# Kernel tuning notes

Measured on AMD Instinct MI355X. Metric: run time of the kernel, lower is better.

The kernel has to match this reference:

```python
import math
import jax, jax.numpy as jnp
from jax import lax
import numpy as np

B, DIM, H, W = 8, 256, 64, 64
D_STATE, D_CONV, EXPAND = 16, 4, 2
D_INNER = EXPAND * DIM
DT_RANK = math.ceil(DIM / 16)
POS_LEN = 16
EPS = 1e-5
GN_GROUPS = 32


def setup_inputs() -> dict:
    key = jax.random.key(0)
    ks = iter(jax.random.split(key, 24))
    rn = lambda shape, s=0.02: jax.random.normal(next(ks), shape, jnp.float32) * s
    inp = {}
    inp["x"] = jax.random.normal(next(ks), (B, DIM, H, W), jnp.float32)
    inp["pos_emb"] = rn((1, DIM, POS_LEN), 1.0)
    inp["ln_g"] = jnp.ones((DIM,), jnp.float32)
    inp["ln_b"] = jnp.zeros((DIM,), jnp.float32)
    inp["m_in_w"] = rn((2, 2 * D_INNER, DIM))
    inp["m_conv_w"] = rn((2, D_INNER, D_CONV), 0.1)
    inp["m_conv_b"] = jnp.zeros((2, D_INNER), jnp.float32)
    inp["m_xproj_w"] = rn((2, DT_RANK + 2 * D_STATE, D_INNER))
    inp["m_dt_w"] = rn((2, D_INNER, DT_RANK), 0.1)
    inp["m_dt_b"] = rn((2, D_INNER), 0.1)
    inp["m_A_log"] = jnp.tile(jnp.log(jnp.arange(1, D_STATE + 1, dtype=jnp.float32))[None, None, :], (2, D_INNER, 1))
    inp["m_D"] = jnp.ones((2, D_INNER), jnp.float32)
    inp["m_out_w"] = rn((2, DIM, D_INNER))
    inp["proj_w"] = rn((DIM, 2 * DIM))
    inp["proj_b"] = jnp.zeros((DIM,), jnp.float32)
    inp["up_dw_w"] = rn((DIM, 1, 3, 3), 0.1)
    inp["up_bn1_g"] = jnp.ones((DIM,), jnp.float32)
    inp["up_bn1_b"] = jnp.zeros((DIM,), jnp.float32)
    inp["up_pw_w"] = rn((DIM, DIM), 0.05)
    inp["up_bn2_g"] = jnp.ones((DIM,), jnp.float32)
    inp["up_bn2_b"] = jnp.zeros((DIM,), jnp.float32)
    inp["down_pw_w"] = rn((DIM, DIM), 0.05)
    inp["down_bn_g"] = jnp.ones((DIM,), jnp.float32)
    inp["down_bn_b"] = jnp.zeros((DIM,), jnp.float32)
    inp["gn_g"] = jnp.ones((DIM,), jnp.float32)
    inp["gn_b"] = jnp.zeros((DIM,), jnp.float32)
    return inp


def reference(x, pos_emb, ln_g, ln_b, m_in_w, m_conv_w, m_conv_b, m_xproj_w, m_dt_w, m_dt_b,
              m_A_log, m_D, m_out_w, proj_w, proj_b, up_dw_w, up_bn1_g, up_bn1_b, up_pw_w,
              up_bn2_g, up_bn2_b, down_pw_w, down_bn_g, down_bn_b, gn_g, gn_b):
    Bx, C, Hh, Ww = x.shape

    def ln(t):  # LayerNorm over last dim (shared self.norm)
        m = jnp.mean(t, -1, keepdims=True)
        v = jnp.mean((t - m) ** 2, -1, keepdims=True)
        return (t - m) * lax.rsqrt(v + EPS) * ln_g + ln_b

    def bn(t, g, b):  # BatchNorm2d in eval mode with default running stats (mean 0, var 1)
        return t * (g / jnp.sqrt(1.0 + EPS))[None, :, None, None] + b[None, :, None, None]

    def gn(t):  # GroupNorm(32, C), shared params (self.bn)
        Bn, Cn, Hn, Wn = t.shape
        tg = t.reshape(Bn, GN_GROUPS, Cn // GN_GROUPS, Hn, Wn)
        m = jnp.mean(tg, (2, 3, 4), keepdims=True)
        v = jnp.mean((tg - m) ** 2, (2, 3, 4), keepdims=True)
        tg = (tg - m) * lax.rsqrt(v + EPS)
        return tg.reshape(Bn, Cn, Hn, Wn) * gn_g[None, :, None, None] + gn_b[None, :, None, None]

    def interp_pos(N):  # F.interpolate(pos_embed, size=N, mode='linear', align_corners=False)
        coords = jnp.maximum((jnp.arange(N, dtype=jnp.float32) + 0.5) * (POS_LEN / N) - 0.5, 0.0)
        i0 = jnp.floor(coords).astype(jnp.int32)
        i1 = jnp.minimum(i0 + 1, POS_LEN - 1)
        wgt = coords - i0.astype(jnp.float32)
        return pos_emb[:, :, i0] * (1.0 - wgt) + pos_emb[:, :, i1] * wgt  # (1,C,N)

    def pe_branch(vals, idx, N):  # vals (B,C,N); indices interp at same size = identity
        t = vals + interp_pos(N) + idx.astype(jnp.float32)
        return ln(jnp.swapaxes(t, 1, 2))  # (B,N,C)

    def mamba(u, d):  # standard mamba_ssm selective scan; u (B,L,C)
        xz = jnp.einsum('blc,ic->bli', u, m_in_w[d])
        xh, zg = jnp.split(xz, 2, -1)
        xc = lax.conv_general_dilated(jnp.swapaxes(xh, 1, 2), m_conv_w[d][:, None, :], (1,),
                                      [(D_CONV - 1, 0)], feature_group_count=D_INNER,
                                      dimension_numbers=('NCH', 'OIH', 'NCH'))
        xc = jnp.swapaxes(jax.nn.silu(xc + m_conv_b[d][None, :, None]), 1, 2)  # (B,L,di)
        dbl = jnp.einsum('bld,ed->ble', xc, m_xproj_w[d])
        dt = dbl[..., :DT_RANK]
        Bm = dbl[..., DT_RANK:DT_RANK + D_STATE]
        Cm = dbl[..., DT_RANK + D_STATE:]
        dt = jax.nn.softplus(jnp.einsum('blr,dr->bld', dt, m_dt_w[d]) + m_dt_b[d])  # (B,L,di)
        A = -jnp.exp(m_A_log[d])  # (di,ds)
        dA = jnp.exp(dt[..., None] * A)  # (B,L,di,ds)
        dBx = dt[..., None] * Bm[:, :, None, :] * xc[..., None]

        def step(h, inps):
            dA_t, dBx_t, C_t = inps
            h = dA_t * h + dBx_t
            return h, jnp.einsum('bds,bs->bd', h, C_t)

        h0 = jnp.zeros((u.shape[0], D_INNER, D_STATE), u.dtype)
        _, ys = lax.scan(step, h0, (jnp.swapaxes(dA, 0, 1), jnp.swapaxes(dBx, 0, 1), jnp.swapaxes(Cm, 0, 1)))
        y = jnp.swapaxes(ys, 0, 1) + xc * m_D[d]
        y = y * jax.nn.silu(zg)
        return jnp.einsum('bld,od->blo', y, m_out_w[d])

    # z branch: depthwise ConvTranspose2d(k3,s2,p1,op1) + BN + ReLU + pw conv + BN, then ReLU6
    z = lax.conv_general_dilated(x, jnp.flip(up_dw_w, (2, 3)), (1, 1), [(1, 2), (1, 2)],
                                 lhs_dilation=(2, 2), feature_group_count=C,
                                 dimension_numbers=('NCHW', 'OIHW', 'NCHW'))  # (B,C,2H,2W)
    z = jax.nn.relu(bn(z, up_bn1_g, up_bn1_b))
    z = jnp.einsum('bchw,oc->bohw', z, up_pw_w)
    z = jnp.clip(bn(z, up_bn2_g, up_bn2_b), 0.0, 6.0)

    col_max = pe_branch(jnp.max(x, 2), jnp.argmax(x, 2), Ww)
    col_min = pe_branch(jnp.min(x, 2), jnp.argmin(x, 2), Ww)
    row_max = pe_branch(jnp.max(x, 3), jnp.argmax(x, 3), Hh)
    row_min = pe_branch(jnp.min(x, 3), jnp.argmin(x, 3), Hh)
    result_max = jnp.concatenate([col_max, row_max], 1)  # (B, W+H, C)
    result_min = jnp.concatenate([col_min, row_min], 1)

    fm_max = ln(mamba(result_max, 0))
    fm_min = ln(mamba(result_min, 0))
    bm_max = ln(mamba(jnp.flip(result_max, 1), 1))
    bm_min = ln(mamba(jnp.flip(result_min, 1), 1))

    res_max = jnp.concatenate([fm_max, jnp.flip(bm_max, 1)], -1) @ proj_w.T + proj_b
    res_min = jnp.concatenate([fm_min, jnp.flip(bm_min, 1)], -1) @ proj_w.T + proj_b
    res_max = ln(res_max)[:, :, None, :]  # (B,L,1,C)
    res_min = ln(res_min)[:, None, :, :]  # (B,1,L,C)

    res = jnp.transpose(res_max + res_min, (0, 3, 1, 2))  # (B,C,L,L), L=H+W=2H
    res = jnp.clip(res + 3.0, 0.0, 6.0) / 6.0 * z  # h_sigmoid gate
    res = gn(res)
    res = jnp.einsum('bchw,oc->bohw', res[:, :, ::2, ::2], down_pw_w)  # pw conv stride 2
    res = bn(res, down_bn_g, down_bn_b)
    res = gn(res)
    res = res + x
    res = gn(res)
    return res
```

## Files before the change

### kernel.cpp

```cpp
#include <hip/hip_runtime.h>
#include <hip/hip_bf16.h>
#include <math.h>

typedef __hip_bfloat16 bf16;
typedef __attribute__((ext_vector_type(8))) short short8_t;
typedef __attribute__((ext_vector_type(4))) short short4_t;
typedef __attribute__((ext_vector_type(4))) float f32x4_t;

#define EPSV 1e-5f
#define BNSC 0.99999500003749968f

__device__ __forceinline__ float bf2f(bf16 v){ return __bfloat162float(v); }
__device__ __forceinline__ bf16 f2bf(float v){ return __float2bfloat16(v); }

__device__ __forceinline__ float blk_sum(float v, float* sm){
  int tid = threadIdx.x;
  #pragma unroll
  for(int o=32;o>0;o>>=1) v += __shfl_down(v, o, 64);
  if((tid&63)==0) sm[tid>>6] = v;
  __syncthreads();
  float s = 0.f;
  int nw = blockDim.x>>6;
  for(int i=0;i<nw;i++) s += sm[i];
  __syncthreads();
  return s;
}

__device__ __forceinline__ float softplusf(float x){
  return (x > 20.f) ? x : __logf(1.f + __expf(x));
}
__device__ __forceinline__ float siluf(float x){
  return x / (1.f + __expf(-x));
}

__global__ void prep_weights(const float* __restrict__ in_w, const float* __restrict__ out_w,
                             const float* __restrict__ pw_w, const float* __restrict__ dpw_w,
                             const float* __restrict__ proj_w,
                             bf16* __restrict__ Winb, bf16* __restrict__ Woutb,
                             bf16* __restrict__ Wub, bf16* __restrict__ Wdb,
                             float* __restrict__ PT, float* __restrict__ gacc){
  int idx = blockIdx.x*256 + threadIdx.x;
  if(idx < 1536) gacc[idx] = 0.f;
  if(idx < 524288){ Winb[idx] = f2bf(in_w[idx]); return; }
  if(idx < 786432){ int i=idx-524288; Woutb[i] = f2bf(out_w[i]); return; }
  if(idx < 851968){ int i=idx-786432; Wub[i] = f2bf(pw_w[i]); return; }
  if(idx < 917504){ int i=idx-851968; Wdb[i] = f2bf(dpw_w[i]); return; }
  int k = idx - 917504;
  int i = k >> 9, j = k & 511;
  PT[j*256 + i] = proj_w[k];
}

__global__ __launch_bounds__(256)
void r1_reduce_pe(const float* __restrict__ x, const float* __restrict__ pe,
                  float* __restrict__ pmax, float* __restrict__ pmin){
  __shared__ float tile[64*65];
  int bc = blockIdx.x;
  int b = bc >> 8, c = bc & 255;
  const float* xp = x + ((size_t)bc << 12);
  for(int i=threadIdx.x; i<4096; i+=256)
    tile[(i>>6)*65 + (i&63)] = xp[i];
  __syncthreads();
  int wv = threadIdx.x >> 6, t = threadIdx.x & 63;
  if(wv >= 2) return;
  float coords = fmaxf((t + 0.5f)*0.25f - 0.5f, 0.f);
  int i0 = (int)floorf(coords);
  int i1 = min(i0+1, 15);
  float wg = coords - (float)i0;
  float pos = pe[c*16+i0]*(1.f-wg) + pe[c*16+i1]*wg;
  if(wv == 0){
    float cmx=-3.4e38f, cmn=3.4e38f; int cax=0, can=0;
    for(int h=0;h<64;h++){
      float v = tile[h*65 + t];
      if(v > cmx){ cmx=v; cax=h; }
      if(v < cmn){ cmn=v; can=h; }
    }
    size_t base_col = ((size_t)b*128 + t)*256 + c;
    pmax[base_col] = cmx + pos + (float)cax;
    pmin[base_col] = cmn + pos + (float)can;
  } else {
    float rmx=-3.4e38f, rmn=3.4e38f; int rax=0, ran=0;
    for(int w=0;w<64;w++){
      float v = tile[t*65 + w];
      if(v > rmx){ rmx=v; rax=w; }
      if(v < rmn){ rmn=v; ran=w; }
    }
    size_t base_row = ((size_t)b*128 + 64 + t)*256 + c;
    pmax[base_row] = rmx + pos + (float)rax;
    pmin[base_row] = rmn + pos + (float)ran;
  }
}

__global__ void ln_rows2(float* __restrict__ bufA, float* __restrict__ bufB,
                         const float* __restrict__ g, const float* __restrict__ bb,
                         bf16* __restrict__ boutA, bf16* __restrict__ boutB){
  __shared__ float sm[8];
  int row = blockIdx.x, t = threadIdx.x;
  float* buf; bf16* bout;
  if(row < 1024){ buf = bufA; bout = boutA; }
  else { buf = bufB; bout = boutB; row -= 1024; }
  float v = buf[(size_t)row*256 + t];
  float m = blk_sum(v, sm) * (1.f/256.f);
  float dv = v - m;
  float var = blk_sum(dv*dv, sm) * (1.f/256.f);
  float r = dv * rsqrtf(var + EPSV) * g[t] + bb[t];
  buf[(size_t)row*256 + t] = r;
  if(bout) bout[(size_t)row*256 + t] = f2bf(r);
}

__global__ __launch_bounds__(256,2)
void m1_mfma(const bf16* __restrict__ ubmax, const bf16* __restrict__ ubmin,
             const bf16* __restrict__ Win, float* __restrict__ xz){
  __shared__ bf16 att[64*264];
  int bx = blockIdx.x;
  int it = bx & 3, lt = (bx>>2)&1, b = (bx>>3)&7, r = bx>>6;
  int d = r & 1;
  const bf16* u = (r < 2) ? ubmax : ubmin;
  int flip = r & 1;
  int t = threadIdx.x;
  {
    int pr = t>>5, cc = (t&31)*8;
    #pragma unroll
    for(int i=0;i<8;i++){
      int p = pr + i*8;
      int l = lt*64 + p;
      int le = flip ? (127 - l) : l;
      short8_t v = *(const short8_t*)((const short*)u + ((size_t)(b*128 + le))*256 + cc);
      *(short8_t*)&att[p*264 + cc] = v;
    }
  }
  __syncthreads();
  int wv = t>>6, lane = t&63, quad = lane>>4, l16 = lane&15;
  int m0 = wv*64;
  f32x4_t acc[4][4];
  #pragma unroll
  for(int ms=0;ms<4;ms++)
    #pragma unroll
    for(int ns=0;ns<4;ns++) acc[ms][ns] = (f32x4_t){0.f,0.f,0.f,0.f};
  const short* wbase = (const short*)Win + ((size_t)d*1024 + it*256)*256;
  for(int k0=0;k0<256;k0+=32){
    short8_t afr[4], bfr[4];
    #pragma unroll
    for(int ms=0;ms<4;ms++)
      afr[ms] = *(const short8_t*)(wbase + (size_t)(m0 + ms*16 + l16)*256 + k0 + quad*8);
    #pragma unroll
    for(int ns=0;ns<4;ns++)
      bfr[ns] = *(const short8_t*)&att[(ns*16 + l16)*264 + k0 + quad*8];
    #pragma unroll
    for(int ms=0;ms<4;ms++)
      #pragma unroll
      for(int ns=0;ns<4;ns++)
        acc[ms][ns] = __builtin_amdgcn_mfma_f32_16x16x32_bf16(afr[ms], bfr[ns], acc[ms][ns], 0,0,0);
  }
  int rb = r*8 + b;
  #pragma unroll
  for(int ns=0;ns<4;ns++){
    int l = lt*64 + ns*16 + l16;
    float* dst = xz + ((size_t)rb*128 + l)*1024 + it*256;
    #pragma unroll
    for(int ms=0;ms<4;ms++){
      int i = m0 + ms*16 + quad*4;
      *(f32x4_t*)(dst + i) = acc[ms][ns];
    }
  }
}

#define LSEG 8
__global__ __launch_bounds__(256)
void m234(const float* __restrict__ xz, const float* __restrict__ cw,
          const float* __restrict__ cb, const float* __restrict__ xproj,
          const float* __restrict__ dtw, const float* __restrict__ dtbias,
          float* __restrict__ xc, float* __restrict__ dbl, float* __restrict__ dt){
  __shared__ float xzs[(LSEG+3)*512];
  __shared__ float xcs[LSEG*512];
  __shared__ float pbuf[LSEG*96];
  __shared__ float dblrow[LSEG*48];
  int bx = blockIdx.x;
  int rb = bx >> 4, seg = bx & 15;
  int l0 = seg * LSEG;
  int d = (rb >> 3) & 1;
  int t = threadIdx.x;
  #pragma unroll
  for(int j=0; j<(LSEG+3)*512/256; j++){
    int i = t + j*256;
    int r = i >> 9, dd = i & 511;
    int ls = l0 - 3 + r;
    xzs[i] = (ls >= 0) ? xz[((size_t)rb*128 + ls)*1024 + dd] : 0.f;
  }
  __syncthreads();
  #pragma unroll
  for(int j=0; j<(LSEG*512)/256; j++){
    int i = t + j*256;
    int lr = i >> 9, dd = i & 511;
    f32x4_t wv = *(const f32x4_t*)(cw + (size_t)(d*512 + dd)*4);
    float s = cb[d*512 + dd];
    s += xzs[(lr+0)*512 + dd]*wv[0];
    s += xzs[(lr+1)*512 + dd]*wv[1];
    s += xzs[(lr+2)*512 + dd]*wv[2];
    s += xzs[(lr+3)*512 + dd]*wv[3];
    s = siluf(s);
    xcs[i] = s;
    xc[((size_t)(rb*128 + l0 + lr))*512 + dd] = s;
  }
  __syncthreads();
  #pragma unroll
  for(int j=0; j<3; j++){
    int id = t + j*256;
    int row = id / 96;
    int rem = id - row*96;
    int e = rem >> 1, part = rem & 1;
    const float* wp = xproj + ((size_t)(d*48 + e)*512) + part*256;
    const float* xr = xcs + row*512 + part*256;
    float s = 0.f;
    #pragma unroll 4
    for(int k4=0; k4<64; k4++){
      f32x4_t wv = *(const f32x4_t*)(wp + k4*4);
      f32x4_t xv = *(const f32x4_t*)(xr + k4*4);
      s += wv[0]*xv[0] + wv[1]*xv[1] + wv[2]*xv[2] + wv[3]*xv[3];
    }
    pbuf[id] = s;
  }
  __syncthreads();
  for(int i=t; i<LSEG*48; i+=256){
    float s = pbuf[2*i] + pbuf[2*i+1];
    dblrow[i] = s;
    int row = i / 48, e = i - row*48;
    dbl[((size_t)(rb*128 + l0 + row))*48 + e] = s;
  }
  __syncthreads();
  #pragma unroll
  for(int j=0; j<(LSEG*512)/256; j++){
    int i = t + j*256;
    int row = i >> 9, dd = i & 511;
    const float* wp = dtw + (size_t)(d*512 + dd)*16;
    const float* dr = dblrow + row*48;
    float s = dtbias[d*512 + dd];
    #pragma unroll
    for(int r4=0; r4<4; r4++){
      f32x4_t wv = *(const f32x4_t*)(wp + r4*4);
      s += dr[r4*4+0]*wv[0] + dr[r4*4+1]*wv[1] + dr[r4*4+2]*wv[2] + dr[r4*4+3]*wv[3];
    }
    dt[((size_t)(rb*128 + l0 + row))*512 + dd] = softplusf(s);
  }
}

__global__ void m5_passA(const float* __restrict__ dt, const float* __restrict__ xc,
                         const float* __restrict__ dbl, const float* __restrict__ Alog,
                         float* __restrict__ P, float* __restrict__ Hl){
  int bx = blockIdx.x;
  int seg = bx & 7, half = (bx>>3)&1, rb = bx>>4;
  int dd = half*256 + threadIdx.x;
  int d = (rb>>3)&1;
  float A[16], h[16], pr[16];
  #pragma unroll
  for(int s=0;s<16;s++){
    A[s] = -__expf(Alog[(size_t)(d*512 + dd)*16 + s]);
    h[s] = 0.f; pr[s] = 1.f;
  }
  int l0 = seg*16;
  for(int l=l0;l<l0+16;l++){
    size_t row = (size_t)rb*128 + l;
    float dtv = dt[row*512 + dd];
    float xcv = xc[row*512 + dd];
    float bx_ = dtv*xcv;
    const float* dr = dbl + row*48;
    #pragma unroll
    for(int s=0;s<16;s++){
      float dA = __expf(dtv*A[s]);
      pr[s] *= dA;
      h[s] = dA*h[s] + bx_*dr[16+s];
    }
  }
  size_t o = ((size_t)(rb*8 + seg)*512 + dd)*16;
  #pragma unroll
  for(int s=0;s<16;s+=4){
    *(f32x4_t*)(P  + o + s) = (f32x4_t){pr[s],pr[s+1],pr[s+2],pr[s+3]};
    *(f32x4_t*)(Hl + o + s) = (f32x4_t){h[s],h[s+1],h[s+2],h[s+3]};
  }
}

__global__ void m5_passB(const float* __restrict__ dt, const float* __restrict__ xc,
                         const float* __restrict__ dbl, const float* __restrict__ xz,
                         const float* __restrict__ Alog, const float* __restrict__ Dp,
                         const float* __restrict__ P, const float* __restrict__ Hl,
                         bf16* __restrict__ ybb){
  int bx = blockIdx.x;
  int seg = bx & 7, half = (bx>>3)&1, rb = bx>>4;
  int dd = half*256 + threadIdx.x;
  int d = (rb>>3)&1;
  float A[16], h[16];
  #pragma unroll
  for(int s=0;s<16;s++){
    A[s] = -__expf(Alog[(size_t)(d*512 + dd)*16 + s]);
    h[s] = 0.f;
  }
  for(int j=0;j<seg;j++){
    size_t o = ((size_t)(rb*8 + j)*512 + dd)*16;
    #pragma unroll
    for(int s=0;s<16;s+=4){
      f32x4_t pv = *(const f32x4_t*)(P + o + s);
      f32x4_t hv = *(const f32x4_t*)(Hl + o + s);
      h[s]   = pv[0]*h[s]   + hv[0];
      h[s+1] = pv[1]*h[s+1] + hv[1];
      h[s+2] = pv[2]*h[s+2] + hv[2];
      h[s+3] = pv[3]*h[s+3] + hv[3];
    }
  }
  float Dv = Dp[d*512 + dd];
  int l0 = seg*16;
  for(int l=l0;l<l0+16;l++){
    size_t row = (size_t)rb*128 + l;
    float dtv = dt[row*512 + dd];
    float xcv = xc[row*512 + dd];
    float zgv = xz[row*1024 + 512 + dd];
    const float* dr = dbl + row*48;
    float bx_ = dtv*xcv;
    float y = 0.f;
    #pragma unroll
    for(int s=0;s<16;s++){
      h[s] = __expf(dtv*A[s])*h[s] + bx_*dr[16+s];
      y += h[s]*dr[32+s];
    }
    ybb[row*512 + dd] = f2bf((y + xcv*Dv) * siluf(zgv));
  }
}

__global__ __launch_bounds__(256,2)
void m6_mfma(const bf16* __restrict__ ybb, const bf16* __restrict__ Wout,
             const float* __restrict__ lng, const float* __restrict__ lnb,
             float* __restrict__ mo){
  __shared__ char smem[64*264*4];
  bf16* ybt = (bf16*)smem;
  float* fbuf = (float*)smem;
  int bx = blockIdx.x;
  int lt = bx & 1, b = (bx>>1)&7, r = bx>>4;
  int d = r & 1, rb = r*8 + b;
  size_t rowbase = (size_t)rb*128 + lt*64;
  int t = threadIdx.x;
  for(int i=t;i<4096;i+=256){
    int row = i>>6, c8 = (i&63)*8;
    short8_t v = *(const short8_t*)((const short*)ybb + (rowbase + row)*512 + c8);
    *(short8_t*)&ybt[row*520 + c8] = v;
  }
  __syncthreads();
  int wv = t>>6, lane = t&63, quad = lane>>4, l16 = lane&15;
  int m0 = wv*64;
  f32x4_t acc[4][4];
  #pragma unroll
  for(int ms=0;ms<4;ms++)
    #pragma unroll
    for(int ns=0;ns<4;ns++) acc[ms][ns] = (f32x4_t){0.f,0.f,0.f,0.f};
  const short* wbase = (const short*)Wout + (size_t)d*256*512;
  for(int k0=0;k0<512;k0+=32){
    short8_t afr[4], bfr[4];
    #pragma unroll
    for(int ms=0;ms<4;ms++)
      afr[ms] = *(const short8_t*)(wbase + (size_t)(m0 + ms*16 + l16)*512 + k0 + quad*8);
    #pragma unroll
    for(int ns=0;ns<4;ns++)
      bfr[ns] = *(const short8_t*)&ybt[(ns*16 + l16)*520 + k0 + quad*8];
    #pragma unroll
    for(int ms=0;ms<4;ms++)
      #pragma unroll
      for(int ns=0;ns<4;ns++)
        acc[ms][ns] = __builtin_amdgcn_mfma_f32_16x16x32_bf16(afr[ms], bfr[ns], acc[ms][ns], 0,0,0);
  }
  __syncthreads();
  #pragma unroll
  for(int ns=0;ns<4;ns++){
    int row = ns*16 + l16;
    #pragma unroll
    for(int ms=0;ms<4;ms++){
      int o = m0 + ms*16 + quad*4;
      *(f32x4_t*)(fbuf + row*264 + o) = acc[ms][ns];
    }
  }
  __syncthreads();
  {
    int row = t >> 2, part = t & 3;
    const float* fr = fbuf + row*264;
    float s = 0.f;
    #pragma unroll 8
    for(int j=0;j<64;j++){
      int col = part*64 + ((j + part*16) & 63);
      s += fr[col];
    }
    s += __shfl_xor(s, 1, 64);
    s += __shfl_xor(s, 2, 64);
    float m = s * (1.f/256.f);
    float q = 0.f;
    #pragma unroll 8
    for(int j=0;j<64;j++){
      int col = part*64 + ((j + part*16) & 63);
      float dv = fr[col] - m;
      q += dv*dv;
    }
    q += __shfl_xor(q, 1, 64);
    q += __shfl_xor(q, 2, 64);
    float rs = rsqrtf(q*(1.f/256.f) + EPSV);
    float* dst = mo + (rowbase + row)*256;
    for(int j=0;j<64;j++){
      int col = part*64 + j;
      dst[col] = (fr[col] - m)*rs*lng[col] + lnb[col];
    }
  }
}

__global__ void m7_proj(const float* __restrict__ mo, const float* __restrict__ PT,
                        const float* __restrict__ pb, const float* __restrict__ lng,
                        const float* __restrict__ lnb, float* __restrict__ resm,
                        float* __restrict__ resn){
  __shared__ float ct[16*512];
  __shared__ float fbuf[16*264];
  int bx = blockIdx.x;
  int tt = bx >> 6, rem = bx & 63, b = rem >> 3, lt = rem & 7;
  int fr_ = tt*2, br = tt*2 + 1;
  for(int i=threadIdx.x;i<16*512;i+=256){
    int lr = i >> 9, k = i & 511;
    int l = lt*16 + lr;
    ct[i] = (k < 256)
      ? mo[(((size_t)(fr_*8+b)*128) + l)*256 + k]
      : mo[(((size_t)(br*8+b)*128) + (127-l))*256 + (k-256)];
  }
  __syncthreads();
  float acc[16];
  #pragma unroll
  for(int q=0;q<16;q++) acc[q] = 0.f;
  int t = threadIdx.x;
  for(int k=0;k<512;k++){
    float pv = PT[(size_t)k*256 + t];
    #pragma unroll
    for(int q=0;q<16;q++) acc[q] += pv * ct[(q<<9) + k];
  }
  float bias = pb[t];
  #pragma unroll
  for(int q=0;q<16;q++) fbuf[q*264 + t] = acc[q] + bias;
  __syncthreads();
  float* dstbuf = tt ? resn : resm;
  if(t < 64){
    int row = t >> 2, part = t & 3;
    const float* fr = fbuf + row*264;
    float s = 0.f;
    for(int j=0;j<64;j++){
      int col = part*64 + ((j + part*16) & 63);
      s += fr[col];
    }
    s += __shfl_xor(s, 1, 64);
    s += __shfl_xor(s, 2, 64);
    float m = s * (1.f/256.f);
    float q = 0.f;
    for(int j=0;j<64;j++){
      int col = part*64 + ((j + part*16) & 63);
      float dv = fr[col] - m;
      q += dv*dv;
    }
    q += __shfl_xor(q, 1, 64);
    q += __shfl_xor(q, 2, 64);
    float rs = rsqrtf(q*(1.f/256.f) + EPSV);
    float* dst = dstbuf + ((size_t)b*128 + lt*16 + row)*256;
    for(int j=0;j<64;j++){
      int col = part*64 + j;
      dst[col] = (fr[col] - m)*rs*lng[col] + lnb[col];
    }
  }
}

__global__ __launch_bounds__(256)
void k1_deconv_T(const float* __restrict__ x, const float* __restrict__ wdw,
                 const float* __restrict__ g1, const float* __restrict__ b1,
                 bf16* __restrict__ zT){
  __shared__ float in[2*64*33];
  __shared__ bf16 ot[64*80];
  int bx = blockIdx.x;
  int cb = bx & 3, half = (bx>>2)&1, h = (bx>>3)&127, b = bx>>10;
  int c0 = cb*64, w0 = half*64, iw0 = w0>>1;
  int h_odd = h & 1;
  int ihA = h_odd ? (h-1)>>1 : h>>1;
  int ihB = (h+1)>>1;
  bool hasB = h_odd && (ihB < 64);
  for(int i = threadIdx.x; i < 4224; i += 256){
    int row = i / 2112;
    int rem = i - row*2112;
    int c = rem / 33;
    int iw = rem - c*33;
    int ihl = row ? ihB : ihA;
    bool valid = (iw0 + iw < 64) && (row == 0 || hasB);
    in[i] = valid ? x[(((size_t)b*256 + c0 + c)<<12) + (ihl<<6) + iw0 + iw] : 0.f;
  }
  __syncthreads();
  int c = threadIdx.x & 63, g = threadIdx.x >> 6;
  const float* wp = wdw + (c0+c)*9;
  int khA3 = h_odd ? 6 : 3;
  float wA0 = wp[khA3], wA1 = wp[khA3+1], wA2 = wp[khA3+2];
  float wB0 = wp[0],    wB1 = wp[1],      wB2 = wp[2];
  float scale = g1[c0+c]*BNSC, bias = b1[c0+c];
  const float* inA = in + c*33;
  const float* inB = in + 2112 + c*33;
  #pragma unroll
  for(int i=0;i<16;i++){
    int wi = g*16 + i;
    float s;
    if(!(i&1)){
      int iw = wi>>1;
      s = inA[iw]*wA1 + inB[iw]*wB1;
    } else {
      int iwa = (wi-1)>>1, iwb = (wi+1)>>1;
      s = inA[iwa]*wA2 + inA[iwb]*wA0 + inB[iwa]*wB2 + inB[iwb]*wB0;
    }
    ot[wi*80 + c] = f2bf(fmaxf(s*scale + bias, 0.f));
  }
  __syncthreads();
  int rr = threadIdx.x >> 3;
  int co = (threadIdx.x & 7) * 8;
  size_t obase = (((size_t)b*16384) + (size_t)h*128 + w0)*256 + c0;
  #pragma unroll
  for(int pass=0; pass<2; pass++){
    int wi = rr + pass*32;
    short8_t v = *(const short8_t*)&ot[wi*80 + co];
    *(short8_t*)((short*)zT + obase + (size_t)wi*256 + co) = v;
  }
}

__global__ __launch_bounds__(256,2)
void k2_mfma(const bf16* __restrict__ zT, const bf16* __restrict__ Wub,
             const float* __restrict__ g2, const float* __restrict__ b2,
             const float* __restrict__ resm, const float* __restrict__ resn,
             bf16* __restrict__ resT){
  __shared__ bf16 zt[128*264];
  int b = blockIdx.y;
  int p0 = blockIdx.x*128;
  int t = threadIdx.x;
  {
    const short* src = (const short*)zT + (((size_t)b*16384 + p0)*256);
    int pr = t>>5;
    int cc = (t&31)*8;
    #pragma unroll
    for(int i=0;i<16;i++){
      int p = pr + i*8;
      short8_t v = *(const short8_t*)(src + (size_t)p*256 + cc);
      *(short8_t*)&zt[p*264 + cc] = v;
    }
  }
  __syncthreads();
  int wv = t>>6, lane = t&63, quad = lane>>4, l16 = lane&15;
  int m0 = wv*64;
  f32x4_t acc[4][8];
  #pragma unroll
  for(int ms=0;ms<4;ms++)
    #pragma unroll
    for(int ns=0;ns<8;ns++) acc[ms][ns] = (f32x4_t){0.f,0.f,0.f,0.f};
  const short* wp = (const short*)Wub + (size_t)(m0 + l16)*256 + quad*8;
  short8_t afr[4];
  #pragma unroll
  for(int ms=0;ms<4;ms++) afr[ms] = *(const short8_t*)(wp + (size_t)ms*16*256);
  for(int k0=0;k0<256;k0+=32){
    short8_t anext[4];
    if(k0 + 32 < 256){
      #pragma unroll
      for(int ms=0;ms<4;ms++)
        anext[ms] = *(const short8_t*)(wp + (size_t)ms*16*256 + k0 + 32);
    }
    short8_t bfr[8];
    #pragma unroll
    for(int ns=0;ns<8;ns++)
      bfr[ns] = *(const short8_t*)&zt[(ns*16 + l16)*264 + k0 + quad*8];
    #pragma unroll
    for(int ms=0;ms<4;ms++)
      #pragma unroll
      for(int ns=0;ns<8;ns++)
        acc[ms][ns] = __builtin_amdgcn_mfma_f32_16x16x32_bf16(afr[ms], bfr[ns], acc[ms][ns], 0,0,0);
    #pragma unroll
    for(int ms=0;ms<4;ms++) afr[ms] = anext[ms];
  }
  __syncthreads();
  #pragma unroll
  for(int ns=0;ns<8;ns++){
    int pl = ns*16 + l16;
    int p = p0 + pl;
    int hh = p>>7, ww = p&127;
    const float* rm = resm + ((size_t)b*128+hh)*256;
    const float* rn = resn + ((size_t)b*128+ww)*256;
    #pragma unroll
    for(int ms=0;ms<4;ms++){
      int o = m0 + ms*16 + quad*4;
      f32x4_t a = acc[ms][ns];
      f32x4_t gv = *(const f32x4_t*)(g2+o);
      f32x4_t bv = *(const f32x4_t*)(b2+o);
      f32x4_t rmv = *(const f32x4_t*)(rm+o);
      f32x4_t rnv = *(const f32x4_t*)(rn+o);
      alignas(8) bf16 ov[4];
      #pragma unroll
      for(int r=0;r<4;r++){
        float zv = a[r]*(gv[r]*BNSC) + bv[r];
        zv = fminf(fmaxf(zv, 0.f), 6.f);
        float gate = fminf(fmaxf(rmv[r]+rnv[r]+3.f, 0.f), 6.f)*(1.f/6.f);
        ov[r] = f2bf(zv*gate);
      }
      *(short4_t*)&zt[pl*264 + o] = *(const short4_t*)ov;
    }
  }
  __syncthreads();
  {
    short* dst = (short*)resT + ((size_t)b*16384 + p0)*256;
    int slot0 = t;
    #pragma unroll
    for(int it=0; it<16; it++){
      int slot = slot0 + it*256;
      int row = slot >> 5;
      int co = (slot & 31)*8;
      short8_t v = *(const short8_t*)&zt[row*264 + co];
      *(short8_t*)(dst + (size_t)row*256 + co) = v;
    }
  }
}

__global__ void gn_stats_pm(const bf16* __restrict__ resT, float* __restrict__ sum,
                            float* __restrict__ ssq){
  __shared__ float ls[256], lq[256];
  int b = blockIdx.y, p0 = blockIdx.x*256;
  int c = threadIdx.x;
  const short* src = (const short*)resT + ((size_t)b*16384 + p0)*256 + c;
  float s=0.f, q=0.f;
  for(int i=0;i<256;i++){
    bf16 raw; *(short*)&raw = src[(size_t)i*256];
    float v = bf2f(raw);
    s += v; q += v*v;
  }
  ls[c]=s; lq[c]=q;
  __syncthreads();
  if(c<32){
    float S=0.f,Q=0.f;
    #pragma unroll
    for(int j=0;j<8;j++){ S+=ls[c*8+j]; Q+=lq[c*8+j]; }
    atomicAdd(&sum[b*32+c], S);
    atomicAdd(&ssq[b*32+c], Q);
  }
}

__global__ __launch_bounds__(256,2)
void k4_mfma(const bf16* __restrict__ resT, const bf16* __restrict__ Wdb,
             const float* __restrict__ gsum1, const float* __restrict__ gssq1,
             const float* __restrict__ gng, const float* __restrict__ gnb,
             const float* __restrict__ dbg, const float* __restrict__ dbb,
             float* __restrict__ t1, float* __restrict__ gsum2, float* __restrict__ gssq2){
  __shared__ bf16 at[128*264];
  __shared__ float sc[256], sb[256];
  __shared__ float stm[32], str[32];
  int b = blockIdx.y;
  int q0 = blockIdx.x*128;
  int t = threadIdx.x;
  if(t < 32){
    float m = gsum1[b*32+t] * (1.f/131072.f);
    float var = gssq1[b*32+t] * (1.f/131072.f) - m*m;
    stm[t] = m;
    str[t] = rsqrtf(var + EPSV);
  }
  __syncthreads();
  {
    int cch = t, g = cch>>3;
    float m = stm[g], rs = str[g];
    float s = rs*gng[cch];
    sc[cch] = s; sb[cch] = gnb[cch] - m*s;
  }
  __syncthreads();
  {
    int pr = t>>5;
    int cc = (t&31)*8;
    #pragma unroll
    for(int i=0;i<16;i++){
      int q = pr + i*8;
      int qq = q0 + q;
      int y = qq>>6, xw = qq&63;
      size_t srow = ((size_t)b*16384 + (size_t)y*256 + xw*2)*256;
      short8_t v = *(const short8_t*)((const short*)resT + srow + cc);
      const bf16* vv = (const bf16*)&v;
      alignas(16) bf16 ov[8];
      #pragma unroll
      for(int j=0;j<8;j++) ov[j] = f2bf(bf2f(vv[j])*sc[cc+j] + sb[cc+j]);
      *(short8_t*)&at[q*264 + cc] = *(const short8_t*)ov;
    }
  }
  __syncthreads();
  int wv = t>>6, lane = t&63, quad = lane>>4, l16 = lane&15;
  int n0 = wv*64;
  f32x4_t acc[8][4];
  #pragma unroll
  for(int ms=0;ms<8;ms++)
    #pragma unroll
    for(int ns=0;ns<4;ns++) acc[ms][ns] = (f32x4_t){0.f,0.f,0.f,0.f};
  const short* wp = (const short*)Wdb + (size_t)(n0 + l16)*256 + quad*8;
  short8_t bfr[4];
  #pragma unroll
  for(int ns=0;ns<4;ns++) bfr[ns] = *(const short8_t*)(wp + (size_t)ns*16*256);
  for(int k0=0;k0<256;k0+=32){
    short8_t bnext[4];
    if(k0 + 32 < 256){
      #pragma unroll
      for(int ns=0;ns<4;ns++)
        bnext[ns] = *(const short8_t*)(wp + (size_t)ns*16*256 + k0 + 32);
    }
    short8_t afr[8];
    #pragma unroll
    for(int ms=0;ms<8;ms++)
      afr[ms] = *(const short8_t*)&at[(ms*16 + l16)*264 + k0 + quad*8];
    #pragma unroll
    for(int ms=0;ms<8;ms++)
      #pragma unroll
      for(int ns=0;ns<4;ns++)
        acc[ms][ns] = __builtin_amdgcn_mfma_f32_16x16x32_bf16(afr[ms], bfr[ns], acc[ms][ns], 0,0,0);
    #pragma unroll
    for(int ns=0;ns<4;ns++) bfr[ns] = bnext[ns];
  }
  #pragma unroll
  for(int ns=0;ns<4;ns++){
    int o = n0 + ns*16 + l16;
    float s2 = dbg[o]*BNSC, bb2 = dbb[o];
    float* dst = t1 + (((size_t)b*256 + o) << 12);
    float s_=0.f, q_=0.f;
    #pragma unroll
    for(int ms=0;ms<8;ms++){
      int ps = q0 + ms*16 + quad*4;
      f32x4_t a = acc[ms][ns];
      f32x4_t ov;
      #pragma unroll
      for(int r=0;r<4;r++){
        ov[r] = a[r]*s2 + bb2;
        s_ += ov[r];
        q_ += ov[r]*ov[r];
      }
      *(f32x4_t*)(dst + ps) = ov;
    }
    #pragma unroll
    for(int msk=1; msk<=4; msk<<=1){
      s_ += __shfl_xor(s_, msk, 64);
      q_ += __shfl_xor(q_, msk, 64);
    }
    s_ += __shfl_xor(s_, 16, 64);
    q_ += __shfl_xor(q_, 16, 64);
    s_ += __shfl_xor(s_, 32, 64);
    q_ += __shfl_xor(q_, 32, 64);
    if(((l16 & 7) == 0) && (quad == 0)){
      atomicAdd(&gsum2[b*32 + (o>>3)], s_);
      atomicAdd(&gssq2[b*32 + (o>>3)], q_);
    }
  }
}

__global__ void k6_gn_add(float* __restrict__ t1, const float* __restrict__ x,
                          const float* __restrict__ gsum2, const float* __restrict__ gssq2,
                          const float* __restrict__ gng, const float* __restrict__ gnb,
                          float* __restrict__ gsum3, float* __restrict__ gssq3){
  __shared__ float sm[8];
  int i4 = blockIdx.x*256 + threadIdx.x;
  int idx = i4 << 2;
  int c = (idx >> 12) & 255, b = idx >> 20, g = c >> 3;
  float m2 = gsum2[b*32+g] * (1.f/32768.f);
  float var = gssq2[b*32+g] * (1.f/32768.f) - m2*m2;
  float rs = rsqrtf(var + EPSV);
  float scl = rs*gng[c], off = gnb[c] - m2*scl;
  f32x4_t tv = *(const f32x4_t*)(t1 + idx);
  f32x4_t xv = *(const f32x4_t*)(x + idx);
  f32x4_t ov;
  float S = 0.f, Q = 0.f;
  #pragma unroll
  for(int r=0;r<4;r++){
    float v = tv[r]*scl + off + xv[r];
    ov[r] = v;
    S += v; Q += v*v;
  }
  *(f32x4_t*)(t1 + idx) = ov;
  S = blk_sum(S, sm);
  Q = blk_sum(Q, sm);
  if(threadIdx.x == 0){
    atomicAdd(&gsum3[b*32 + g], S);
    atomicAdd(&gssq3[b*32 + g], Q);
  }
}

__global__ void k8_gn_out(const float* __restrict__ t1, const float* __restrict__ gsum3,
                          const float* __restrict__ gssq3, const float* __restrict__ gng,
                          const float* __restrict__ gnb, float* __restrict__ out){
  int i4 = blockIdx.x*256 + threadIdx.x;
  int idx = i4 << 2;
  int c = (idx >> 12) & 255, b = idx >> 20, g = c >> 3;
  float m = gsum3[b*32+g] * (1.f/32768.f);
  float var = gssq3[b*32+g] * (1.f/32768.f) - m*m;
  float rs = rsqrtf(var + EPSV);
  float scl = rs*gng[c], off = gnb[c] - m*scl;
  f32x4_t tv = *(const f32x4_t*)(t1 + idx);
  f32x4_t ov;
  #pragma unroll
  for(int r=0;r<4;r++) ov[r] = tv[r]*scl + off;
  *(f32x4_t*)(out + idx) = ov;
}

extern "C" void kernel_launch(void* const* d_in, const int* in_sizes, int n_in,
                              void* d_out, int out_size, void* d_ws, size_t ws_size,
                              hipStream_t stream){
  const float* x      = (const float*)d_in[0];
  const float* pos    = (const float*)d_in[1];
  const float* ln_g   = (const float*)d_in[2];
  const float* ln_b   = (const float*)d_in[3];
  const float* in_w   = (const float*)d_in[4];
  const float* conv_w = (const float*)d_in[5];
  const float* conv_b = (const float*)d_in[6];
  const float* xproj  = (const float*)d_in[7];
  const float* dt_w   = (const float*)d_in[8];
  const float* dt_b   = (const float*)d_in[9];
  const float* A_log  = (const float*)d_in[10];
  const float* Dp     = (const float*)d_in[11];
  const float* out_w  = (const float*)d_in[12];
  const float* proj_w = (const float*)d_in[13];
  const float* proj_b = (const float*)d_in[14];
  const float* dw_w   = (const float*)d_in[15];
  const float* bn1g   = (const float*)d_in[16];
  const float* bn1b   = (const float*)d_in[17];
  const float* pw_w   = (const float*)d_in[18];
  const float* bn2g   = (const float*)d_in[19];
  const float* bn2b   = (const float*)d_in[20];
  const float* dpw_w  = (const float*)d_in[21];
  const float* dbng   = (const float*)d_in[22];
  const float* dbnb   = (const float*)d_in[23];
  const float* gng    = (const float*)d_in[24];
  const float* gnb    = (const float*)d_in[25];
  float* out = (float*)d_out;

  float* ws = (float*)d_ws;
  bf16*  resT = (bf16*)ws;
  bf16*  zT   = (bf16*)(ws + 16777216);
  float* scanP = ws + 16777216;
  float* scanH = ws + 16777216 + 2097152;
  float* zone = ws + 33554432;
  float* xz   = zone;
  float* xc   = xz  + 4194304;
  float* dbl  = xc  + 2097152;
  float* dtb  = dbl + 196608;
  bf16*  ybb  = (bf16*)(dtb + 2097152);
  float* t1   = zone;
  float* mo   = zone + 9633792;
  float* resm = mo   + 1048576;
  float* resn = resm + 262144;
  float* pmax = resn + 262144;
  float* pmin = pmax + 262144;
  float* PT   = pmin + 262144;
  bf16*  ubmax= (bf16*)(PT + 131072);
  bf16*  ubmin= (bf16*)(PT + 131072 + 131072);
  bf16*  Winb = (bf16*)(PT + 131072 + 262144);
  bf16*  Woutb= (bf16*)(PT + 131072 + 524288);
  bf16*  Wub  = (bf16*)(PT + 131072 + 655360);
  bf16*  Wdb  = (bf16*)(PT + 131072 + 688128);
  float* gacc = PT + 131072 + 720896;
  float* gsum1 = gacc,        *gssq1 = gacc + 256;
  float* gsum2 = gacc + 512,  *gssq2 = gacc + 768;
  float* gsum3 = gacc + 1024, *gssq3 = gacc + 1280;

  prep_weights<<<4096,256,0,stream>>>(in_w, out_w, pw_w, dpw_w, proj_w,
                                      Winb, Woutb, Wub, Wdb, PT, gacc);

  r1_reduce_pe<<<2048,256,0,stream>>>(x, pos, pmax, pmin);
  ln_rows2<<<2048,256,0,stream>>>(pmax, pmin, ln_g, ln_b, ubmax, ubmin);

  m1_mfma<<<256,256,0,stream>>>(ubmax, ubmin, Winb, xz);
  m234<<<512,256,0,stream>>>(xz, conv_w, conv_b, xproj, dt_w, dt_b, xc, dbl, dtb);
  m5_passA<<<512,256,0,stream>>>(dtb, xc, dbl, A_log, scanP, scanH);
  m5_passB<<<512,256,0,stream>>>(dtb, xc, dbl, xz, A_log, Dp, scanP, scanH, ybb);
  m6_mfma<<<64,256,0,stream>>>(ybb, Woutb, ln_g, ln_b, mo);
  m7_proj<<<128,256,0,stream>>>(mo, PT, proj_b, ln_g, ln_b, resm, resn);

  k1_deconv_T<<<8192,256,0,stream>>>(x, dw_w, bn1g, bn1b, zT);
  k2_mfma<<<dim3(128,8),256,0,stream>>>(zT, Wub, bn2g, bn2b, resm, resn, resT);
  gn_stats_pm<<<dim3(64,8),256,0,stream>>>(resT, gsum1, gssq1);

  k4_mfma<<<dim3(32,8),256,0,stream>>>(resT, Wdb, gsum1, gssq1,
                                       gng, gnb, dbng, dbnb, t1, gsum2, gssq2);

  k6_gn_add<<<8192,256,0,stream>>>(t1, x, gsum2, gssq2, gng, gnb, gsum3, gssq3);
  k8_gn_out<<<8192,256,0,stream>>>(t1, gsum3, gssq3, gng, gnb, out);
}
```

Measured before the change: 510.4 us.

## Fuse GroupNorm statistics into k2 GEMM epilogue and halve k2 tile

The per-group sum and sum-of-squares for the first GroupNorm are now accumulated in the k2 epilogue, using wave shuffles, shared-memory atomics and one global atomic per group per block. This removes the separate gn_stats_pm kernel, which re-read the whole bf16 resT tensor from memory. k2's tile also drops from 128 to 64 pixels per block, with launch bounds raised to 4 blocks per CU and the grid doubled, to lower LDS and register use and raise occupancy. The cost is more weight fragment reloads per pixel, and the statistics are now taken from fp32 values rather than the rounded bf16 outputs.

```diff
diff --git a/kernel.cpp b/kernel.cpp
--- a/kernel.cpp
+++ b/kernel.cpp
@@ -520,21 +520,23 @@
   }
 }
 
-__global__ __launch_bounds__(256,2)
+__global__ __launch_bounds__(256,4)
 void k2_mfma(const bf16* __restrict__ zT, const bf16* __restrict__ Wub,
              const float* __restrict__ g2, const float* __restrict__ b2,
              const float* __restrict__ resm, const float* __restrict__ resn,
-             bf16* __restrict__ resT){
-  __shared__ bf16 zt[128*264];
+             bf16* __restrict__ resT, float* __restrict__ gsum1, float* __restrict__ gssq1){
+  __shared__ bf16 zt[64*264];
+  __shared__ float gn_s[32], gn_q[32];
   int b = blockIdx.y;
-  int p0 = blockIdx.x*128;
+  int p0 = blockIdx.x*64;
   int t = threadIdx.x;
+  if(t < 32){ gn_s[t] = 0.f; gn_q[t] = 0.f; }
   {
     const short* src = (const short*)zT + (((size_t)b*16384 + p0)*256);
     int pr = t>>5;
     int cc = (t&31)*8;
     #pragma unroll
-    for(int i=0;i<16;i++){
+    for(int i=0;i<8;i++){
       int p = pr + i*8;
       short8_t v = *(const short8_t*)(src + (size_t)p*256 + cc);
       *(short8_t*)&zt[p*264 + cc] = v;
@@ -543,11 +545,11 @@
   __syncthreads();
   int wv = t>>6, lane = t&63, quad = lane>>4, l16 = lane&15;
   int m0 = wv*64;
-  f32x4_t acc[4][8];
+  f32x4_t acc[4][4];
   #pragma unroll
   for(int ms=0;ms<4;ms++)
     #pragma unroll
-    for(int ns=0;ns<8;ns++) acc[ms][ns] = (f32x4_t){0.f,0.f,0.f,0.f};
+    for(int ns=0;ns<4;ns++) acc[ms][ns] = (f32x4_t){0.f,0.f,0.f,0.f};
   const short* wp = (const short*)Wub + (size_t)(m0 + l16)*256 + quad*8;
   short8_t afr[4];
   #pragma unroll
@@ -559,21 +561,24 @@
       for(int ms=0;ms<4;ms++)
         anext[ms] = *(const short8_t*)(wp + (size_t)ms*16*256 + k0 + 32);
     }
-    short8_t bfr[8];
-    #pragma unroll
-    for(int ns=0;ns<8;ns++)
+    short8_t bfr[4];
+    #pragma unroll
+    for(int ns=0;ns<4;ns++)
       bfr[ns] = *(const short8_t*)&zt[(ns*16 + l16)*264 + k0 + quad*8];
     #pragma unroll
     for(int ms=0;ms<4;ms++)
       #pragma unroll
-      for(int ns=0;ns<8;ns++)
+      for(int ns=0;ns<4;ns++)
         acc[ms][ns] = __builtin_amdgcn_mfma_f32_16x16x32_bf16(afr[ms], bfr[ns], acc[ms][ns], 0,0,0);
     #pragma unroll
     for(int ms=0;ms<4;ms++) afr[ms] = anext[ms];
   }
   __syncthreads();
-  #pragma unroll
-  for(int ns=0;ns<8;ns++){
+  float sg[4], qg[4];
+  #pragma unroll
+  for(int ms=0;ms<4;ms++){ sg[ms]=0.f; qg[ms]=0.f; }
+  #pragma unroll
+  for(int ns=0;ns<4;ns++){
     int pl = ns*16 + l16;
     int p = p0 + pl;
     int hh = p>>7, ww = p&127;
@@ -593,46 +598,42 @@
         float zv = a[r]*(gv[r]*BNSC) + bv[r];
         zv = fminf(fmaxf(zv, 0.f), 6.f);
         float gate = fminf(fmaxf(rmv[r]+rnv[r]+3.f, 0.f), 6.f)*(1.f/6.f);
-        ov[r] = f2bf(zv*gate);
+        float vo = zv*gate;
+        ov[r] = f2bf(vo);
+        sg[ms] += vo;
+        qg[ms] += vo*vo;
       }
       *(short4_t*)&zt[pl*264 + o] = *(const short4_t*)ov;
     }
   }
-  __syncthreads();
+  #pragma unroll
+  for(int ms=0;ms<4;ms++){
+    float S = sg[ms], Q = qg[ms];
+    S += __shfl_xor(S, 1, 64);  Q += __shfl_xor(Q, 1, 64);
+    S += __shfl_xor(S, 2, 64);  Q += __shfl_xor(Q, 2, 64);
+    S += __shfl_xor(S, 4, 64);  Q += __shfl_xor(Q, 4, 64);
+    S += __shfl_xor(S, 8, 64);  Q += __shfl_xor(Q, 8, 64);
+    if(l16 == 0){
+      int o = m0 + ms*16 + quad*4;
+      atomicAdd(&gn_s[o>>3], S);
+      atomicAdd(&gn_q[o>>3], Q);
+    }
+  }
+  __syncthreads();
+  if(t < 32){
+    atomicAdd(&gsum1[b*32 + t], gn_s[t]);
+    atomicAdd(&gssq1[b*32 + t], gn_q[t]);
+  }
   {
     short* dst = (short*)resT + ((size_t)b*16384 + p0)*256;
-    int slot0 = t;
-    #pragma unroll
-    for(int it=0; it<16; it++){
-      int slot = slot0 + it*256;
+    #pragma unroll
+    for(int it=0; it<8; it++){
+      int slot = t + it*256;
       int row = slot >> 5;
       int co = (slot & 31)*8;
       short8_t v = *(const short8_t*)&zt[row*264 + co];
       *(short8_t*)(dst + (size_t)row*256 + co) = v;
     }
-  }
-}
-
-__global__ void gn_stats_pm(const bf16* __restrict__ resT, float* __restrict__ sum,
-                            float* __restrict__ ssq){
-  __shared__ float ls[256], lq[256];
-  int b = blockIdx.y, p0 = blockIdx.x*256;
-  int c = threadIdx.x;
-  const short* src = (const short*)resT + ((size_t)b*16384 + p0)*256 + c;
-  float s=0.f, q=0.f;
-  for(int i=0;i<256;i++){
-    bf16 raw; *(short*)&raw = src[(size_t)i*256];
-    float v = bf2f(raw);
-    s += v; q += v*v;
-  }
-  ls[c]=s; lq[c]=q;
-  __syncthreads();
-  if(c<32){
-    float S=0.f,Q=0.f;
-    #pragma unroll
-    for(int j=0;j<8;j++){ S+=ls[c*8+j]; Q+=lq[c*8+j]; }
-    atomicAdd(&sum[b*32+c], S);
-    atomicAdd(&ssq[b*32+c], Q);
   }
 }
 
@@ -867,8 +868,8 @@
   m7_proj<<<128,256,0,stream>>>(mo, PT, proj_b, ln_g, ln_b, resm, resn);
 
   k1_deconv_T<<<8192,256,0,stream>>>(x, dw_w, bn1g, bn1b, zT);
-  k2_mfma<<<dim3(128,8),256,0,stream>>>(zT, Wub, bn2g, bn2b, resm, resn, resT);
-  gn_stats_pm<<<dim3(64,8),256,0,stream>>>(resT, gsum1, gssq1);
+  k2_mfma<<<dim3(256,8),256,0,stream>>>(zT, Wub, bn2g, bn2b, resm, resn, resT,
+                                        gsum1, gssq1);
 
   k4_mfma<<<dim3(32,8),256,0,stream>>>(resT, Wdb, gsum1, gssq1,
                                        gng, gnb, dbng, dbnb, t1, gsum2, gssq2);
```

Result: no change. 517.3 us (+1.4%).
